# Optimization experiments

Hardware: AMD Instinct MI355X
Metric: run time of the kernel (lower is better)

The kernel has to match this reference:

```python
import jax, jax.numpy as jnp
import numpy as np

IN_CH = 1280
NUM_HEADS = 8
DIM_DOWN = 5
CUT_RATE = 4
SCALE = (IN_CH // NUM_HEADS) ** -0.5  # faithful to original: uses in_ch//num_heads


def setup_inputs() -> dict:
    key = jax.random.key(0)
    ks = jax.random.split(key, 5)
    B, N = 4, 4096
    C = IN_CH // DIM_DOWN  # 256
    x = jax.random.normal(ks[0], (B, N, IN_CH), dtype=jnp.float32)
    Wd = jax.random.normal(ks[1], (IN_CH, C), dtype=jnp.float32) * (IN_CH ** -0.5)
    Wqkv = jax.random.normal(ks[2], (C, 3 * C), dtype=jnp.float32) * (C ** -0.5)
    Wup = jax.random.normal(ks[3], (C, IN_CH), dtype=jnp.float32) * (C ** -0.5)
    bup = jnp.zeros((IN_CH,), dtype=jnp.float32)
    return {"x": x, "Wd": Wd, "Wqkv": Wqkv, "Wup": Wup, "bup": bup}


def reference(x, Wd, Wqkv, Wup, bup):
    # dim-down projection (dropout is identity at rate 0 / eval)
    h = x @ Wd                                  # [B, N, C]
    B, N, C = h.shape
    H = NUM_HEADS
    hd = C // H
    blk = N // CUT_RATE
    qkv = (h @ Wqkv).reshape(B, N, 3, H, hd)
    qkv = jnp.transpose(qkv, (2, 0, 3, 1, 4))   # [3, B, H, N, hd]
    q, k, v = qkv[0], qkv[1], qkv[2]
    # block-diagonal local attention: split N into CUT_RATE independent chunks
    q = q.reshape(B, H, CUT_RATE, blk, hd)
    k = k.reshape(B, H, CUT_RATE, blk, hd)
    v = v.reshape(B, H, CUT_RATE, blk, hd)
    attn = jnp.einsum('bhcqd,bhckd->bhcqk', q, k) * SCALE
    attn = jax.nn.softmax(attn, axis=-1)
    o = jnp.einsum('bhcqk,bhckd->bhcqd', attn, v)
    # torch cat over chunks along token dim, then merge heads: [B, N, C]
    o = jnp.transpose(o, (0, 2, 3, 1, 4)).reshape(B, N, C)
    return o @ Wup + bup
```

## Files before the change

kernel.cpp:

```cpp
#include <hip/hip_runtime.h>

typedef unsigned short u16;
typedef unsigned int u32;
typedef u16 u16x4 __attribute__((ext_vector_type(4)));
typedef u16 u16x8 __attribute__((ext_vector_type(8)));
typedef __bf16 bf16x8 __attribute__((ext_vector_type(8)));
typedef float f32x4 __attribute__((ext_vector_type(4)));

__device__ __forceinline__ u16 f2bf(float f) {
  union { float f; unsigned u; } c; c.f = f;
  unsigned u = c.u;
  return (u16)((u + 0x7fff + ((u >> 16) & 1)) >> 16);
}

__device__ __forceinline__ float fexp2(float x) {
  float r; asm("v_exp_f32 %0, %1" : "=v"(r) : "v"(x)); return r;
}

__device__ __forceinline__ u32 cvtpk(float lo, float hi) {
  u32 r;
  asm("v_cvt_pk_bf16_f32 %0, %1, %2" : "=v"(r) : "v"(lo), "v"(hi));
  return r;
}

__device__ __forceinline__ void lds16(const u16* g, u16* l) {
  __builtin_amdgcn_global_load_lds(
      (const __attribute__((address_space(1))) unsigned int*)g,
      (__attribute__((address_space(3))) unsigned int*)l, 16, 0, 0);
}

#define CEXP (0.07905694150420949f * 1.4426950408889634f)

#define BAR()  do { asm volatile("" ::: "memory"); \
                    __builtin_amdgcn_s_barrier(); \
                    asm volatile("" ::: "memory"); } while (0)
#define VMC(n) asm volatile("s_waitcnt vmcnt(" #n ")" ::: "memory")

#define PREP_W (1280 * 256 + 768 * 256 + 1280 * 256)

__global__ __launch_bounds__(256)
void prep_w(const float* __restrict__ Wd, const float* __restrict__ Wqkv,
            const float* __restrict__ Wup,
            u16* __restrict__ WdC, u16* __restrict__ WqkvT,
            u16* __restrict__ WupT) {
  int id = blockIdx.x * 256 + threadIdx.x;
  if (id < 1280 * 256) {
    WdC[id] = f2bf(Wd[id]);
    return;
  }
  id -= 1280 * 256;
  if (id < 768 * 256) {
    int n = id >> 8, c = id & 255;
    float v = Wqkv[(size_t)c * 768 + n];
    if (n < 256) v *= CEXP;
    WqkvT[id] = f2bf(v);
    return;
  }
  id -= 768 * 256;
  if (id < 1280 * 256) {
    int n = id >> 8, c = id & 255;
    WupT[id] = f2bf(Wup[(size_t)c * 1280 + n]);
  }
}

__global__ __launch_bounds__(256)
void wpt_xcast(const u16* __restrict__ WqkvT, const u16* __restrict__ WdC,
               u16* __restrict__ WpT,
               const float* __restrict__ X, u16* __restrict__ Xb, int n8)
{
  __shared__ u16 As[128][64];
  __shared__ u16 Bs[128][64];

  if (blockIdx.x >= 60) {
    int id = (blockIdx.x - 60) * 256 + threadIdx.x;
    if (id < n8) {
      const float4* src = (const float4*)(X + (size_t)id * 8);
      float4 lo = src[0], hi = src[1];
      u16x8 v;
      v[0]=f2bf(lo.x); v[1]=f2bf(lo.y); v[2]=f2bf(lo.z); v[3]=f2bf(lo.w);
      v[4]=f2bf(hi.x); v[5]=f2bf(hi.y); v[6]=f2bf(hi.z); v[7]=f2bf(hi.w);
      *(u16x8*)(Xb + (size_t)id * 8) = v;
    }
    return;
  }

  const int tid  = threadIdx.x;
  const int wave = tid >> 6, lane = tid & 63;
  const int quad = lane >> 4, l16 = lane & 15;
  const int rsw  = l16 & 7;
  const int ssw  = ((lane & 7) ^ (lane >> 3)) << 3;
  const int band = blockIdx.x / 10, nblk = blockIdx.x % 10;
  const int m0 = band * 128, n0 = nblk * 128;
  const int wr = (wave >> 1) * 64, wc = (wave & 1) * 64;
  const int K = 256, N = 1280;

  f32x4 acc[4][4];
#pragma unroll
  for (int i = 0; i < 4; i++)
#pragma unroll
    for (int j = 0; j < 4; j++) acc[i][j] = f32x4{0.f, 0.f, 0.f, 0.f};

  for (int k0 = 0; k0 < K; k0 += 64) {
#pragma unroll
    for (int it = 0; it < 4; it++) {
      int r0 = wave * 32 + it * 8;
      lds16(&WqkvT[(size_t)(m0 + r0 + (lane >> 3)) * K + k0 + ssw],
            &As[r0][0] + lane * 8);
      lds16(&WdC[(size_t)(n0 + r0 + (lane >> 3)) * K + k0 + ssw],
            &Bs[r0][0] + lane * 8);
    }
    __syncthreads();
#pragma unroll
    for (int ks = 0; ks < 64; ks += 32) {
      bf16x8 af[4], bfr[4];
#pragma unroll
      for (int i = 0; i < 4; i++)
        af[i] = *(const bf16x8*)&As[wr + i * 16 + l16][(((ks >> 3) + quad) ^ rsw) << 3];
#pragma unroll
      for (int j = 0; j < 4; j++)
        bfr[j] = *(const bf16x8*)&Bs[wc + j * 16 + l16][(((ks >> 3) + quad) ^ rsw) << 3];
#pragma unroll
      for (int i = 0; i < 4; i++)
#pragma unroll
        for (int j = 0; j < 4; j++)
          acc[i][j] = __builtin_amdgcn_mfma_f32_16x16x32_bf16(af[i], bfr[j], acc[i][j], 0, 0, 0);
    }
    __syncthreads();
  }

#pragma unroll
  for (int i = 0; i < 4; i++)
#pragma unroll
    for (int j = 0; j < 4; j++) {
      int col = n0 + wc + j * 16 + l16;
#pragma unroll
      for (int r = 0; r < 4; r++) {
        int row = m0 + wr + i * 16 + quad * 4 + r;
        WpT[(size_t)row * N + col] = f2bf(acc[i][j][r]);
      }
    }
}

template <int AF32>
__global__ __launch_bounds__(256)
void gemm_bt(const void* __restrict__ Av,
             const u16* __restrict__ BT,
             u16* __restrict__ Cb, float* __restrict__ Cf,
             const float* __restrict__ bias,
             int M, int N, int K)
{
  __shared__ u16 As[128][64];
  __shared__ u16 Bs[128][64];
  const int tid  = threadIdx.x;
  const int wave = tid >> 6, lane = tid & 63;
  const int quad = lane >> 4, l16 = lane & 15;
  const int rsw  = l16 & 7;
  const int ssw  = ((lane & 7) ^ (lane >> 3)) << 3;

  const int nb = N >> 7, mb = M >> 7;
  int band, nblk;
  if ((mb & 7) == 0) {
    int xcd = blockIdx.x & 7, slot = blockIdx.x >> 3;
    band = xcd + 8 * (slot / nb);
    nblk = slot % nb;
  } else {
    band = blockIdx.x / nb;
    nblk = blockIdx.x % nb;
  }
  const int m0 = band * 128, n0 = nblk * 128;
  const int wr = (wave >> 1) * 64, wc = (wave & 1) * 64;
  const u16*   A16 = (const u16*)Av;
  const float* A32 = (const float*)Av;

  f32x4 acc[4][4];
#pragma unroll
  for (int i = 0; i < 4; i++)
#pragma unroll
    for (int j = 0; j < 4; j++) acc[i][j] = f32x4{0.f, 0.f, 0.f, 0.f};

  for (int k0 = 0; k0 < K; k0 += 64) {
    if constexpr (AF32) {
#pragma unroll
      for (int it = 0; it < 4; it++) {
        int idx = tid + it * 256;
        int r = idx >> 3;
        const float* src = &A32[(size_t)(m0 + r) * K + k0 + ((idx & 7) << 3)];
        float4 lo = *(const float4*)src;
        float4 hi = *(const float4*)(src + 4);
        u16x8 v;
        v[0]=f2bf(lo.x); v[1]=f2bf(lo.y); v[2]=f2bf(lo.z); v[3]=f2bf(lo.w);
        v[4]=f2bf(hi.x); v[5]=f2bf(hi.y); v[6]=f2bf(hi.z); v[7]=f2bf(hi.w);
        *(u16x8*)&As[r][((idx & 7) ^ (r & 7)) << 3] = v;
      }
#pragma unroll
      for (int it = 0; it < 4; it++) {
        int r0 = wave * 32 + it * 8;
        lds16(&BT[(size_t)(n0 + r0 + (lane >> 3)) * K + k0 + ssw],
              &Bs[r0][0] + lane * 8);
      }
    } else {
#pragma unroll
      for (int it = 0; it < 4; it++) {
        int r0 = wave * 32 + it * 8;
        lds16(&A16[(size_t)(m0 + r0 + (lane >> 3)) * K + k0 + ssw],
              &As[r0][0] + lane * 8);
        lds16(&BT[(size_t)(n0 + r0 + (lane >> 3)) * K + k0 + ssw],
              &Bs[r0][0] + lane * 8);
      }
    }
    __syncthreads();
#pragma unroll
    for (int ks = 0; ks < 64; ks += 32) {
      bf16x8 af[4], bfr[4];
#pragma unroll
      for (int i = 0; i < 4; i++)
        af[i] = *(const bf16x8*)&As[wr + i * 16 + l16][(((ks >> 3) + quad) ^ rsw) << 3];
#pragma unroll
      for (int j = 0; j < 4; j++)
        bfr[j] = *(const bf16x8*)&Bs[wc + j * 16 + l16][(((ks >> 3) + quad) ^ rsw) << 3];
#pragma unroll
      for (int i = 0; i < 4; i++)
#pragma unroll
        for (int j = 0; j < 4; j++)
          acc[i][j] = __builtin_amdgcn_mfma_f32_16x16x32_bf16(af[i], bfr[j], acc[i][j], 0, 0, 0);
    }
    __syncthreads();
  }

#pragma unroll
  for (int i = 0; i < 4; i++) {
#pragma unroll
    for (int j = 0; j < 4; j++) {
      int col = n0 + wc + j * 16 + l16;
      float bv = bias ? bias[col] : 0.0f;
#pragma unroll
      for (int r = 0; r < 4; r++) {
        int row = m0 + wr + i * 16 + quad * 4 + r;
        float v = acc[i][j][r] + bv;
        if (Cf) Cf[(size_t)row * N + col] = v;
        else    Cb[(size_t)row * N + col] = f2bf(v);
      }
    }
  }
}

#define LDA_(d, ib) { _Pragma("unroll") for (int i = 0; i < 4; i++) \
  _Pragma("unroll") for (int ks = 0; ks < 2; ks++) \
    af[i*2+ks] = *(const bf16x8*)&As[d][wm][(ib+i)*16 + l16][((ks*4+quad) ^ rsw) << 3]; }

#define LDB_(d, dst, jp) { _Pragma("unroll") for (int j = 0; j < 2; j++) \
  _Pragma("unroll") for (int ks = 0; ks < 2; ks++) \
    dst[j*2+ks] = *(const bf16x8*)&Bs[d][bh][br + (jp*2+j)*16 + l16][((ks*4+quad) ^ rsw) << 3]; }

#define MM_(ib, jp, breg) { __builtin_amdgcn_s_setprio(1); \
  _Pragma("unroll") for (int i = 0; i < 4; i++) \
  _Pragma("unroll") for (int j = 0; j < 2; j++) \
  _Pragma("unroll") for (int ks = 0; ks < 2; ks++) \
    acc[ib+i][jp*2+j] = __builtin_amdgcn_mfma_f32_16x16x32_bf16( \
        af[i*2+ks], breg[j*2+ks], acc[ib+i][jp*2+j], 0, 0, 0); \
  __builtin_amdgcn_s_setprio(0); }

__global__ __launch_bounds__(512, 2)
void gemm_qkv(const u16* __restrict__ A16, const u16* __restrict__ BT,
              u16* __restrict__ qT, u16* __restrict__ kT,
              u16* __restrict__ vT, int M, int N, int K)
{
  __shared__ __align__(16) u16 SH[2][2][2][128][64];
  auto& As = SH[0];
  auto& Bs = SH[1];
  const int tid  = threadIdx.x;
  const int wave = tid >> 6, lane = tid & 63;
  const int quad = lane >> 4, l16 = lane & 15;
  const int wm = wave >> 2, wn = wave & 3;
  const int bh = wn >> 1, br = (wn & 1) * 64;
  const int rsw = l16 & 7;

  const int nb = N >> 8;
  const int xcd = blockIdx.x & 7, slot = blockIdx.x >> 3;
  const int band = xcd + 8 * (slot / nb);
  const int nblk = slot % nb;
  const int m0 = band * 256, n0 = nblk * 256;
  const int NT = K >> 6;

  const int srow = tid >> 3;
  const int scol = ((tid & 7) ^ (srow & 7)) << 3;

  auto stageA = [&](int t, int h) {
    const int d = t & 1;
    const size_t g = (size_t)(m0 + h * 128 + srow) * K + (t << 6) + scol;
    lds16(&A16[g], &As[d][h][0][0] + tid * 8);
    lds16(&A16[g + (size_t)64 * K], &As[d][h][64][0] + tid * 8);
  };
  auto stageB = [&](int t, int h) {
    const int d = t & 1;
    const size_t g = (size_t)(n0 + h * 128 + srow) * K + (t << 6) + scol;
    lds16(&BT[g], &Bs[d][h][0][0] + tid * 8);
    lds16(&BT[g + (size_t)64 * K], &Bs[d][h][64][0] + tid * 8);
  };

  bf16x8 af[8], b0[4], b1[4];
  f32x4 acc[8][4];
#pragma unroll
  for (int i = 0; i < 8; i++)
#pragma unroll
    for (int j = 0; j < 4; j++) acc[i][j] = f32x4{0.f, 0.f, 0.f, 0.f};

  stageA(0, 0); stageA(0, 1); stageB(0, 0); stageB(0, 1); stageA(1, 0);
  VMC(2);
  BAR();

  const int nIter = NT >> 1;
  for (int it = 0; it < nIter; ++it) {
    const int t0 = it * 2, t1 = t0 + 1;
    const bool more  = (t0 + 2 < NT);
    const bool more1 = (t1 + 2 < NT);

    LDA_(0, 0); LDB_(0, b0, 0);
    stageA(t1, 1);
    BAR(); MM_(0, 0, b0); BAR();
    LDB_(0, b1, 1);
    stageB(t1, 0);
    BAR(); MM_(0, 1, b1); BAR();
    LDA_(0, 4);
    stageB(t1, 1);
    BAR(); MM_(4, 1, b1); BAR();
    if (more) stageA(t0 + 2, 0);
    BAR(); MM_(4, 0, b0);
    if (more) { VMC(2); } else { VMC(0); }
    BAR();

    LDA_(1, 0); LDB_(1, b0, 0);
    if (more) stageA(t0 + 2, 1);
    BAR(); MM_(0, 0, b0); BAR();
    LDB_(1, b1, 1);
    if (more) stageB(t0 + 2, 0);
    BAR(); MM_(0, 1, b1); BAR();
    LDA_(1, 4);
    if (more) stageB(t0 + 2, 1);
    BAR(); MM_(4, 1, b1); BAR();
    if (more1) stageA(t1 + 2, 0);
    BAR(); MM_(4, 0, b0);
    if (it + 1 < nIter) {
      if (more1) { VMC(2); } else { VMC(0); }
      BAR();
    }
  }

  const int b_ = m0 >> 12, chunk_ = (m0 >> 10) & 3;
  const int ghb = (b_ * 4 + chunk_) * 8;

  if (n0 == 512) {
    u16* T = &SH[0][0][0][0][0];
    BAR();
#pragma unroll
    for (int i = 0; i < 8; i++)
#pragma unroll
      for (int j = 0; j < 4; j++) {
        const int vcol = wn * 64 + j * 16 + l16;
        const int tok4 = (wm * 128 + i * 16 + quad * 4) ^ ((vcol & 7) << 2);
        uint2 w;
        w.x = cvtpk(acc[i][j][0], acc[i][j][1]);
        w.y = cvtpk(acc[i][j][2], acc[i][j][3]);
        *(uint2*)&T[vcol * 256 + tok4] = w;
      }
    __syncthreads();
    const int ktb = (m0 & 1023) >> 6;
    const int s   = tid & 7;
    const int hd0 = tid >> 3;
#pragma unroll
    for (int u = 0; u < 4; u++) {
      const int hd = u * 64 + hd0;
      const int head = hd >> 5, d = hd & 31;
      const int x = (hd & 7) << 2;
      const size_t gb = (size_t)(ghb + head) * 32768 + (size_t)d * 1024 + s * 8;
#pragma unroll
      for (int kt4 = 0; kt4 < 4; kt4++) {
        const int base = kt4 * 64 + ((s >> 2) << 5) + ((s & 3) << 2);
        u16x4 lo = *(const u16x4*)&T[hd * 256 + (base ^ x)];
        u16x4 hi = *(const u16x4*)&T[hd * 256 + ((base + 16) ^ x)];
        u16x8 o8;
        o8[0]=lo[0]; o8[1]=lo[1]; o8[2]=lo[2]; o8[3]=lo[3];
        o8[4]=hi[0]; o8[5]=hi[1]; o8[6]=hi[2]; o8[7]=hi[3];
        *(u16x8*)&vT[gb + (size_t)(ktb + kt4) * 64] = o8;
      }
    }
  } else {
    u16* P = (n0 == 0) ? qT : kT;
    const int tic0 = (m0 & 1023) + wm * 128 + quad * 4;
#pragma unroll
    for (int i = 0; i < 8; i++)
#pragma unroll
      for (int j = 0; j < 4; j++) {
        const int c255 = wn * 64 + j * 16 + l16;
        const int head = c255 >> 5, d = c255 & 31;
        u16* Pg = P + (size_t)(ghb + head) * 32768 + d;
#pragma unroll
        for (int r = 0; r < 4; r++) {
          const int tic = tic0 + i * 16 + r;
          Pg[(size_t)tic * 32] = f2bf(acc[i][j][r]);
        }
      }
  }
}

__global__ __launch_bounds__(256)
void repack_fb(const u16* __restrict__ qkv, u16* __restrict__ qT,
               u16* __restrict__ kT, u16* __restrict__ vT)
{
  int id = blockIdx.x * 256 + threadIdx.x;
  int tok = id >> 3, head = id & 7;
  int b = tok >> 12, chunk = (tok >> 10) & 3, tic = tok & 1023;
  int gh = (b * 4 + chunk) * 8 + head;
  int kt = tic >> 6, k64 = tic & 63, b32 = k64 >> 5, k32 = k64 & 31;
  int s = b32 * 4 + ((k32 >> 2) & 3);
  int j = (k32 & 3) | ((k32 >> 4) << 2);
  size_t src = (size_t)tok * 768 + head * 32;
  for (int d = 0; d < 32; d++) {
    qT[(size_t)gh * 32768 + (size_t)tic * 32 + d] = qkv[src + d];
    kT[(size_t)gh * 32768 + (size_t)tic * 32 + d] = qkv[src + 256 + d];
    vT[(size_t)gh * 32768 + (size_t)d * 1024 + kt * 64 + s * 8 + j] = qkv[src + 512 + d];
  }
}

__global__ __launch_bounds__(256)
void attn_kernel(const u16* __restrict__ qT, const u16* __restrict__ kT,
                 const u16* __restrict__ vT, u16* __restrict__ o)
{
  __shared__ __align__(16) u16 Ks[4][64][32];
  __shared__ __align__(16) u16 VTs[4][32][64];

  const int tid  = threadIdx.x;
  const int wave = tid >> 6, lane = tid & 63;
  const int quad = lane >> 4, l16 = lane & 15;
  const int gid   = blockIdx.x;
  const int qb    = gid >> 7;
  const int g     = gid & 127;
  const int head  = g >> 4;
  const int chunk = (g >> 2) & 3;
  const int b     = g & 3;
  const int gh    = (b * 4 + chunk) * 8 + head;
  const size_t rowbase = (size_t)b * 4096 + chunk * 1024;
  const int tok0 = qb * 128 + wave * 32;

  const int vr   = tid >> 3;
  const int vs   = tid & 7;
  const int vsl  = (vs ^ (vr & 7)) << 3;
  const size_t vbase = (size_t)gh * 32768 + (size_t)vr * 1024 + vsl;
  const size_t kbase = (size_t)gh * 32768;

  auto stageKV = [&](int kb, int buf) {
    lds16(&kT[kbase + kb * 2048 + tid * 8], &Ks[buf][0][0] + tid * 8);
    lds16(&vT[vbase + (size_t)kb * 64], &VTs[buf][0][0] + tid * 8);
  };

  stageKV(0, 0);

  bf16x8 qf[2];
#pragma unroll
  for (int qt = 0; qt < 2; qt++)
    qf[qt] = *(const bf16x8*)&qT[kbase + (size_t)(tok0 + qt * 16 + l16) * 32 + quad * 8];

  stageKV(1, 1);

  bf16x8 onesb;
  {
    union { u16x8 u; bf16x8 v; } c;
#pragma unroll
    for (int i = 0; i < 8; i++) c.u[i] = 0x3F80;
    onesb = c.v;
  }

  f32x4 Oacc[2][2], Osum[2];
#pragma unroll
  for (int qt = 0; qt < 2; qt++) {
    Osum[qt] = f32x4{0.f, 0.f, 0.f, 0.f};
#pragma unroll
    for (int nd = 0; nd < 2; nd++) Oacc[qt][nd] = f32x4{0.f, 0.f, 0.f, 0.f};
  }

  VMC(2);
  BAR();

  for (int kb = 0; kb < 16; kb++) {
    const int cur = kb & 3;
    if (kb + 2 < 16) stageKV(kb + 2, (kb + 2) & 3);

    bf16x8 kf[4];
#pragma unroll
    for (int kt = 0; kt < 4; kt++)
      kf[kt] = *(const bf16x8*)&Ks[cur][kt * 16 + l16][quad * 8];

    f32x4 ST[4][2];
    __builtin_amdgcn_s_setprio(1);
#pragma unroll
    for (int kt = 0; kt < 4; kt++)
#pragma unroll
      for (int qt = 0; qt < 2; qt++)
        ST[kt][qt] = __builtin_amdgcn_mfma_f32_16x16x32_bf16(kf[kt], qf[qt], f32x4{0.f,0.f,0.f,0.f}, 0, 0, 0);
    __builtin_amdgcn_s_setprio(0);

    u32 pw[2][4][2];
#pragma unroll
    for (int qt = 0; qt < 2; qt++)
#pragma unroll
      for (int kt = 0; kt < 4; kt++) {
        float p0 = fexp2(ST[kt][qt][0]);
        float p1 = fexp2(ST[kt][qt][1]);
        float p2 = fexp2(ST[kt][qt][2]);
        float p3 = fexp2(ST[kt][qt][3]);
        pw[qt][kt][0] = cvtpk(p0, p1);
        pw[qt][kt][1] = cvtpk(p2, p3);
      }

#pragma unroll
    for (int ks = 0; ks < 2; ks++) {
      bf16x8 vf[2];
#pragma unroll
      for (int nd = 0; nd < 2; nd++)
        vf[nd] = *(const bf16x8*)&VTs[cur][nd * 16 + l16][((ks * 4 + quad) ^ (l16 & 7)) << 3];
      __builtin_amdgcn_s_setprio(1);
#pragma unroll
      for (int qt = 0; qt < 2; qt++) {
        union { u32 w[4]; bf16x8 v; } pu;
        pu.w[0] = pw[qt][2 * ks][0];
        pu.w[1] = pw[qt][2 * ks][1];
        pu.w[2] = pw[qt][2 * ks + 1][0];
        pu.w[3] = pw[qt][2 * ks + 1][1];
#pragma unroll
        for (int nd = 0; nd < 2; nd++)
          Oacc[qt][nd] = __builtin_amdgcn_mfma_f32_16x16x32_bf16(pu.v, vf[nd], Oacc[qt][nd], 0, 0, 0);
        Osum[qt] = __builtin_amdgcn_mfma_f32_16x16x32_bf16(pu.v, onesb, Osum[qt], 0, 0, 0);
      }
      __builtin_amdgcn_s_setprio(0);
    }

    if (kb < 15) {
      if (kb + 2 < 16) { VMC(2); } else { VMC(0); }
      BAR();
    }
  }

#pragma unroll
  for (int qt = 0; qt < 2; qt++)
#pragma unroll
    for (int r = 0; r < 4; r++) {
      float inv = 1.0f / Osum[qt][r];
      size_t row = rowbase + tok0 + qt * 16 + quad * 4 + r;
#pragma unroll
      for (int nd = 0; nd < 2; nd++) {
        int col = head * 32 + nd * 16 + l16;
        o[row * 256 + col] = f2bf(Oacc[qt][nd][r] * inv);
      }
    }
}

extern "C" void kernel_launch(void* const* d_in, const int* in_sizes, int n_in,
                              void* d_out, int out_size, void* d_ws, size_t ws_size,
                              hipStream_t stream)
{
  const float* x    = (const float*)d_in[0];
  const float* Wd   = (const float*)d_in[1];
  const float* Wqkv = (const float*)d_in[2];
  const float* Wup  = (const float*)d_in[3];
  const float* bup  = (const float*)d_in[4];
  float* out = (float*)d_out;

  const int M = 4 * 4096;
  const size_t PANEL = (size_t)128 * 32768;

  u16* WdC   = (u16*)d_ws;
  u16* WqkvT = WdC   + 1280 * 256;
  u16* WupT  = WqkvT + 768 * 256;
  u16* WpT   = WupT  + 1280 * 256;
  u16* qT    = WpT   + 768 * 1280;
  u16* kT    = qT    + PANEL;
  u16* vT    = kT    + PANEL;
  u16* ob    = vT    + PANEL;
  u16* xb    = ob    + (size_t)M * 256;

  const size_t need = ((size_t)(1280*256 + 768*256 + 1280*256 + 768*1280)
                       + (size_t)M * (768 + 256 + 1280)) * sizeof(u16);
  const bool use_xb = ws_size >= need;

  prep_w<<<(PREP_W + 255) / 256, 256, 0, stream>>>(
      Wd, Wqkv, Wup, WdC, WqkvT, WupT);

  const int n8 = use_xb ? (M * 1280 / 8) : 0;
  wpt_xcast<<<60 + (n8 + 255) / 256, 256, 0, stream>>>(
      WqkvT, WdC, WpT, x, xb, n8);

  const u16 *aq, *ak, *av;
  if (use_xb) {
    gemm_qkv<<<dim3((768 / 256) * (M / 256)), 512, 0, stream>>>(
        xb, WpT, qT, kT, vT, M, 768, 1280);
    aq = qT; ak = kT; av = vT;
  } else {
    u16* qkv = qT;
    gemm_bt<1><<<dim3((768 / 128) * (M / 128)), 256, 0, stream>>>(
        (const void*)x, WpT, qkv, nullptr, nullptr, M, 768, 1280);
    u16* s0 = (u16*)d_out;
    repack_fb<<<(M * 8) / 256, 256, 0, stream>>>(qkv, s0, s0 + PANEL, s0 + 2 * PANEL);
    aq = s0; ak = s0 + PANEL; av = s0 + 2 * PANEL;
  }

  attn_kernel<<<dim3(1024), 256, 0, stream>>>(aq, ak, av, ob);

  gemm_bt<0><<<dim3((1280 / 128) * (M / 128)), 256, 0, stream>>>(
      (const void*)ob, WupT, nullptr, out, bup, M, 1280, 256);
}
```

Before: 250.2 us.

## Restructure GEMM main loop to prefetch full tiles two iterations ahead

Replaces the hand-interleaved two-tile unrolled loop, which staged one half-tile at a time, with a simple per-tile loop. Each iteration issues the whole A and B staging for tile t+2 into the double buffer just read, and waits with a deeper vmcnt so more global-to-LDS loads are in flight. This is meant to hide more memory latency and simplify the schedule. The risk is that the stage writes for t+2 target the same LDS buffer being read for tile t, which depends on barrier placement, and the loads are less evenly spread across the MFMA phases.

```diff
diff --git a/kernel.cpp b/kernel.cpp
--- a/kernel.cpp
+++ b/kernel.cpp
@@ -305,43 +305,26 @@
 #pragma unroll
     for (int j = 0; j < 4; j++) acc[i][j] = f32x4{0.f, 0.f, 0.f, 0.f};
 
-  stageA(0, 0); stageA(0, 1); stageB(0, 0); stageB(0, 1); stageA(1, 0);
-  VMC(2);
+  stageA(0, 0); stageA(0, 1); stageB(0, 0); stageB(0, 1);
+  stageA(1, 0); stageA(1, 1); stageB(1, 0); stageB(1, 1);
+  VMC(8);
   BAR();
 
-  const int nIter = NT >> 1;
-  for (int it = 0; it < nIter; ++it) {
-    const int t0 = it * 2, t1 = t0 + 1;
-    const bool more  = (t0 + 2 < NT);
-    const bool more1 = (t1 + 2 < NT);
-
-    LDA_(0, 0); LDB_(0, b0, 0);
-    stageA(t1, 1);
+  for (int t = 0; t < NT; ++t) {
+    const int d = t & 1;
+    const bool pf = (t + 2 < NT);
+
+    LDA_(d, 0); LDB_(d, b0, 0);
     BAR(); MM_(0, 0, b0); BAR();
-    LDB_(0, b1, 1);
-    stageB(t1, 0);
+    LDB_(d, b1, 1);
     BAR(); MM_(0, 1, b1); BAR();
-    LDA_(0, 4);
-    stageB(t1, 1);
+    LDA_(d, 4);
+    if (pf) { stageB(t + 2, 0); stageB(t + 2, 1); }
     BAR(); MM_(4, 1, b1); BAR();
-    if (more) stageA(t0 + 2, 0);
+    if (pf) { stageA(t + 2, 0); stageA(t + 2, 1); }
     BAR(); MM_(4, 0, b0);
-    if (more) { VMC(2); } else { VMC(0); }
-    BAR();
-
-    LDA_(1, 0); LDB_(1, b0, 0);
-    if (more) stageA(t0 + 2, 1);
-    BAR(); MM_(0, 0, b0); BAR();
-    LDB_(1, b1, 1);
-    if (more) stageB(t0 + 2, 0);
-    BAR(); MM_(0, 1, b1); BAR();
-    LDA_(1, 4);
-    if (more) stageB(t0 + 2, 1);
-    BAR(); MM_(4, 1, b1); BAR();
-    if (more1) stageA(t1 + 2, 0);
-    BAR(); MM_(4, 0, b0);
-    if (it + 1 < nIter) {
-      if (more1) { VMC(2); } else { VMC(0); }
+    if (t + 1 < NT) {
+      if (pf) { VMC(8); } else { VMC(0); }
       BAR();
     }
   }
```

Measured after the change: 250.9 us. No clear change (+0.3%).
